# Kernel optimization log

Measured on AMD Instinct MI355X. Metric: run time of the kernel, lower is better.

The kernel has to match this reference:

```python
import jax, jax.numpy as jnp
import numpy as np

N = 8192      # nodes
E = 131072    # edges (avg degree 16)
MUL = 128     # multiplicity of 0e and 1o channels
A = 10        # node_attrs (element one-hot) dim
RB = 8        # radial basis size
INV_SQRT3 = 0.5773502691896258  # w3j normalization for l=1 paths


def _lin0(x, W):
    # e3nn-style Linear on scalar (l=0) channels, 1/sqrt(fan_in) normalization
    return (x @ W) / jnp.sqrt(jnp.asarray(W.shape[0], x.dtype))


def _lin1(v, W):
    # e3nn-style Linear on l=1 channels: mixes multiplicities, acts identically on the 3 components
    return jnp.einsum('nuc,uw->nwc', v, W) / jnp.sqrt(jnp.asarray(W.shape[0], v.dtype))


def setup_inputs() -> dict:
    key = jax.random.key(0)
    ks = jax.random.split(key, 26)
    f32 = jnp.float32
    w = lambda k, s: jax.random.normal(k, s, f32)
    D_EF = RB + 2 * MUL  # 264: radial basis + source + target scalar embeddings
    return {
        'node_attrs': jax.random.uniform(ks[0], (N, A), f32),
        'node_feats': w(ks[1], (N, 4 * MUL)),
        'edge_attrs': w(ks[2], (E, 4)),
        'edge_feats': jax.random.uniform(ks[3], (E, RB), f32),
        'edge_index': jax.random.randint(ks[4], (2, E), 0, N, jnp.int32),
        'W_skip_s': w(ks[5], (MUL, MUL)), 'W_skip_v': w(ks[6], (MUL, MUL)),
        'W_up_s': w(ks[7], (MUL, MUL)), 'W_up_v': w(ks[8], (MUL, MUL)),
        'W_src': w(ks[9], (A, MUL)), 'W_tgt': w(ks[10], (A, MUL)),
        'W_r0': w(ks[11], (D_EF, 64)), 'W_r1': w(ks[12], (64, 64)),
        'W_r2': w(ks[13], (64, 64)), 'W_r3': w(ks[14], (64, 4 * MUL)),
        'W_d0': w(ks[15], (D_EF, 64)), 'W_d1': w(ks[16], (64, 1)),
        'W1_s': w(ks[17], (2 * MUL, 2 * MUL)), 'W1_v': w(ks[18], (2 * MUL, MUL)),
        'Wres_s': w(ks[19], (MUL, 2 * MUL)), 'Wres_v': w(ks[20], (MUL, MUL)),
        'W2_s': w(ks[21], (MUL, MUL)), 'W2_v': w(ks[22], (MUL, MUL)),
        'alpha': jnp.asarray(20.0, f32), 'beta': jnp.asarray(0.0, f32),
    }


def reference(node_attrs, node_feats, edge_attrs, edge_feats, edge_index,
              W_skip_s, W_skip_v, W_up_s, W_up_v, W_src, W_tgt,
              W_r0, W_r1, W_r2, W_r3, W_d0, W_d1,
              W1_s, W1_v, Wres_s, Wres_v, W2_s, W2_v, alpha, beta):
    n = node_feats.shape[0]
    s = node_feats[:, :MUL]                       # [N,128] 0e
    v = node_feats[:, MUL:].reshape(n, MUL, 3)    # [N,128,3] 1o
    # skip_tp: Linear(node_feats -> hidden)
    sc = jnp.concatenate([_lin0(s, W_skip_s), _lin1(v, W_skip_v).reshape(n, -1)], axis=-1)
    # linear_up: Linear(node_feats -> edge_irreps)
    us, uv = _lin0(s, W_up_s), _lin1(v, W_up_v)
    # source/target scalar embeddings from node_attrs
    src_e = _lin0(node_attrs, W_src)
    tgt_e = _lin0(node_attrs, W_tgt)
    snd, rcv = edge_index[0], edge_index[1]
    ef = jnp.concatenate([edge_feats, src_e[snd], tgt_e[rcv]], axis=-1)   # [E,264]
    # radial MLP -> per-edge tensor product weights
    h = jax.nn.silu(_lin0(ef, W_r0))
    h = jax.nn.silu(_lin0(h, W_r1))
    h = jax.nn.silu(_lin0(h, W_r2))
    tpw = _lin0(h, W_r3)                          # [E, 4*128]
    # edge density -> per-node density via scatter-sum
    d = jax.nn.silu(_lin0(ef, W_d0))
    edge_density = jnp.tanh(_lin0(d, W_d1) ** 2)  # [E,1]
    density = jax.ops.segment_sum(edge_density, rcv, num_segments=n)      # [N,1]
    # sparse CG tensor product (uvu), paths: 0x0->0e, 0x1->1o, 1x0->1o, 1x1->0e
    xs, xv = us[snd], uv[snd]                     # gather sender features
    y0, y1 = edge_attrs[:, 0], edge_attrs[:, 1:4]
    w1, w2, w3, w4 = jnp.split(tpw, 4, axis=-1)
    m0a = w1 * xs * y0[:, None]                                          # 0e x 0e -> 0e
    m0b = w4 * jnp.einsum('euc,ec->eu', xv, y1) * INV_SQRT3              # 1o x 1o -> 0e
    m1a = (w2 * xs)[:, :, None] * y1[:, None, :] * INV_SQRT3             # 0e x 1o -> 1o
    m1b = w3[:, :, None] * xv * y0[:, None, None] * INV_SQRT3            # 1o x 0e -> 1o
    mid_s = jnp.concatenate([m0a, m0b], axis=1)   # [E,256] irreps_mid scalars
    mid_v = jnp.concatenate([m1a, m1b], axis=1)   # [E,256,3] irreps_mid vectors
    msg_s = jax.ops.segment_sum(mid_s, rcv, num_segments=n)
    msg_v = jax.ops.segment_sum(mid_v, rcv, num_segments=n)
    # linear_1 + learned density normalization
    denom = density * beta + alpha                # [N,1]
    m_s = _lin0(msg_s, W1_s) / denom
    m_v = _lin1(msg_v, W1_v) / denom[..., None]
    # linear_res on up-projected node feats
    m_s = m_s + _lin0(us, Wres_s)                 # [N,256]: 128 scalars + 128 gates
    m_v = m_v + _lin1(uv, Wres_v)                 # [N,128,3]
    # Gate: silu on scalars, sigmoid gates on vectors
    out_s = jax.nn.silu(m_s[:, :MUL])
    out_v = m_v * jax.nn.sigmoid(m_s[:, MUL:])[:, :, None]
    # linear_2
    f_s = _lin0(out_s, W2_s)
    f_v = _lin1(out_v, W2_v)
    # reshape_irreps -> [N, mul, 1+3]
    out = jnp.concatenate([f_s[:, :, None], f_v], axis=2)
    return out, sc
```

## Files before the change

### kernel.cpp

```cpp
#include <hip/hip_runtime.h>

#define NN 8192
#define EE 131072
#define MUL 128
#define AA 10
#define RB 8
#define DEF 264
#define INV_SQRT3 0.5773502691896258f
#define INV_SQRT128 0.08838834764831845f
#define INV_SQRT10 0.31622776601683794f
#define INV_SQRT264 0.06154574548966636f

typedef __attribute__((ext_vector_type(8))) short short8;
typedef __attribute__((ext_vector_type(4))) float floatx4;

#define WS_XQ     ((size_t)0)
#define WS_USB    (WS_XQ    + (size_t)NN*256)
#define WS_UVB    (WS_USB   + (size_t)NN*64)
#define WS_SRC    (WS_UVB   + (size_t)NN*192)
#define WS_TGT    (WS_SRC   + (size_t)NN*64)
#define WS_MSGSB  (WS_TGT   + (size_t)NN*64)
#define WS_MSGVB  (WS_MSGSB + (size_t)NN*128)
#define WS_GATE   (WS_MSGVB + (size_t)NN*384)
#define WS_COUNTS (WS_GATE  + (size_t)NN*128)
#define WS_OFFS   (WS_COUNTS+ (size_t)NN)
#define WS_CURSOR (WS_OFFS  + (size_t)(NN+4))
#define WS_POS    (WS_CURSOR+ (size_t)NN)
#define WS_META   (WS_POS   + (size_t)EE)
#define WS_TPW    (WS_META  + (size_t)EE*8)
#define WS_WB     (WS_TPW   + (size_t)EE*256)
#define WS_WP     (WS_WB    + (size_t)152*256)
#define WS_WN     (WS_WP    + (size_t)352*256)

__device__ __forceinline__ float silu_f(float x) { return x / (1.f + __expf(-x)); }
__device__ __forceinline__ float sigm_f(float x) { return 1.f / (1.f + __expf(-x)); }

__device__ __forceinline__ unsigned short f2bf(float x) {
    union { float f; unsigned u; } uf; uf.f = x;
    unsigned r = uf.u + 0x7FFFu + ((uf.u >> 16) & 1u);
    return (unsigned short)(r >> 16);
}

__global__ __launch_bounds__(256) void csr_count(
    const int* __restrict__ edge_index, int* __restrict__ counts)
{
    int e = blockIdx.x * 256 + threadIdx.x;
    atomicAdd(&counts[edge_index[EE + e]], 1);
}

__global__ __launch_bounds__(1024) void csr_scan(
    const int* __restrict__ counts, int* __restrict__ offs, int* __restrict__ cursor)
{
    __shared__ int sums[1024];
    const int t = threadIdx.x;
    int local[8];
    int s = 0;
#pragma unroll
    for (int k = 0; k < 8; ++k) { local[k] = s; s += counts[t * 8 + k]; }
    sums[t] = s;
    __syncthreads();
    for (int d = 1; d < 1024; d <<= 1) {
        int v = (t >= d) ? sums[t - d] : 0;
        __syncthreads();
        sums[t] += v;
        __syncthreads();
    }
    int base = (t > 0) ? sums[t - 1] : 0;
#pragma unroll
    for (int k = 0; k < 8; ++k) {
        offs[t * 8 + k] = base + local[k];
        cursor[t * 8 + k] = base + local[k];
    }
    if (t == 1023) offs[8192] = sums[1023];
}

__global__ __launch_bounds__(256) void csr_scatter(
    const int* __restrict__ edge_index, int* __restrict__ cursor, int* __restrict__ pos)
{
    int e = blockIdx.x * 256 + threadIdx.x;
    pos[e] = atomicAdd(&cursor[edge_index[EE + e]], 1);
}

__global__ __launch_bounds__(256) void swizzle_weights(
    const float* __restrict__ Wr0, const float* __restrict__ Wd0,
    const float* __restrict__ Wr1, const float* __restrict__ Wr2,
    const float* __restrict__ Wr3, unsigned short* __restrict__ WBall)
{
    int fid = blockIdx.x * 256 + threadIdx.x;
    int lane = fid & 63;
    int frag = fid >> 6;
    int k0 = (lane >> 4) * 8;
    int n0 = lane & 15;
    unsigned short o[8];

    if (frag < 72) {
        int kt = frag >> 3, nt = frag & 7;
        int n = nt * 16 + n0;
#pragma unroll
        for (int j = 0; j < 8; ++j) {
            int k = kt * 32 + k0 + j;
            float v = 0.f;
            if (k < 264) v = ((n < 64) ? Wr0[k * 64 + n] : Wd0[k * 64 + (n - 64)]) * INV_SQRT264;
            o[j] = f2bf(v);
        }
    } else if (frag < 80) {
        int fl = frag - 72;
        int kt = fl >> 2, nt = fl & 3;
        int n = nt * 16 + n0;
#pragma unroll
        for (int j = 0; j < 8; ++j)
            o[j] = f2bf(Wr1[(kt * 32 + k0 + j) * 64 + n] * 0.125f);
    } else if (frag < 88) {
        int fl = frag - 80;
        int kt = fl >> 2, nt = fl & 3;
        int n = nt * 16 + n0;
#pragma unroll
        for (int j = 0; j < 8; ++j)
            o[j] = f2bf(Wr2[(kt * 32 + k0 + j) * 64 + n] * 0.125f);
    } else {
        int fl = frag - 88;
        int kt = fl >> 5, nt = fl & 31;
        int n = nt * 16 + n0;
        int q = n >> 6;
        float sc = (q < 2) ? 0.125f : 0.125f * INV_SQRT3;
#pragma unroll
        for (int j = 0; j < 8; ++j)
            o[j] = f2bf(Wr3[(kt * 32 + k0 + j) * 512 + n] * sc);
    }
    uint4 pk;
    pk.x = (unsigned)o[0] | ((unsigned)o[1] << 16);
    pk.y = (unsigned)o[2] | ((unsigned)o[3] << 16);
    pk.z = (unsigned)o[4] | ((unsigned)o[5] << 16);
    pk.w = (unsigned)o[6] | ((unsigned)o[7] << 16);
    *(uint4*)(WBall + (size_t)fid * 8) = pk;
}

__global__ __launch_bounds__(256) void swizzle_post(
    const float* __restrict__ W1s, const float* __restrict__ W1v,
    const float* __restrict__ Wrs, const float* __restrict__ Wrv,
    const float* __restrict__ W2s, const float* __restrict__ W2v,
    unsigned short* __restrict__ WPall)
{
    int fid = blockIdx.x * 256 + threadIdx.x;
    int lane = fid & 63;
    int frag = fid >> 6;
    int k0 = (lane >> 4) * 8;
    int n0 = lane & 15;
    unsigned short o[8];

    if (frag < 192) {
        int kt = frag >> 4, nt = frag & 15;
        int n = nt * 16 + n0;
#pragma unroll
        for (int j = 0; j < 8; ++j) {
            int k = kt * 32 + k0 + j;
            float v = (k < 256) ? W1s[k * 256 + n] * 0.0625f
                                : Wrs[(k - 256) * 256 + n] * INV_SQRT128;
            o[j] = f2bf(v);
        }
    } else if (frag < 288) {
        int fl = frag - 192;
        int kt = fl >> 3, nt = fl & 7;
        int n = nt * 16 + n0;
#pragma unroll
        for (int j = 0; j < 8; ++j) {
            int k = kt * 32 + k0 + j;
            float v = (k < 256) ? W1v[k * 128 + n] * 0.0625f
                                : Wrv[(k - 256) * 128 + n] * INV_SQRT128;
            o[j] = f2bf(v);
        }
    } else if (frag < 320) {
        int fl = frag - 288;
        int kt = fl >> 3, nt = fl & 7;
        int n = nt * 16 + n0;
#pragma unroll
        for (int j = 0; j < 8; ++j)
            o[j] = f2bf(W2s[(kt * 32 + k0 + j) * 128 + n] * INV_SQRT128);
    } else {
        int fl = frag - 320;
        int kt = fl >> 3, nt = fl & 7;
        int n = nt * 16 + n0;
#pragma unroll
        for (int j = 0; j < 8; ++j)
            o[j] = f2bf(W2v[(kt * 32 + k0 + j) * 128 + n] * INV_SQRT128);
    }
    uint4 pk;
    pk.x = (unsigned)o[0] | ((unsigned)o[1] << 16);
    pk.y = (unsigned)o[2] | ((unsigned)o[3] << 16);
    pk.z = (unsigned)o[4] | ((unsigned)o[5] << 16);
    pk.w = (unsigned)o[6] | ((unsigned)o[7] << 16);
    *(uint4*)(WPall + (size_t)fid * 8) = pk;
}

__global__ __launch_bounds__(256) void swizzle_node(
    const float* __restrict__ Wss, const float* __restrict__ Wus,
    const float* __restrict__ Wsv, const float* __restrict__ Wuv,
    const float* __restrict__ Wsrc, const float* __restrict__ Wtgt,
    unsigned short* __restrict__ WN)
{
    int fid = blockIdx.x * 256 + threadIdx.x;
    int lane = fid & 63;
    int frag = fid >> 6;
    int k0 = (lane >> 4) * 8;
    int m0 = lane & 15;
    unsigned short o[8];

    if (frag < 128) {
        int g = frag >> 5;
        int fl = frag & 31;
        int kt = fl >> 3, mt = fl & 7;
        const float* W = (g == 0) ? Wss : (g == 1) ? Wus : (g == 2) ? Wsv : Wuv;
        int m = mt * 16 + m0;
#pragma unroll
        for (int j = 0; j < 8; ++j)
            o[j] = f2bf(W[(kt * 32 + k0 + j) * 128 + m] * INV_SQRT128);
    } else {
        int g = (frag - 128) >> 3;
        int mt = frag & 7;
        const float* W = g ? Wtgt : Wsrc;
        int m = mt * 16 + m0;
#pragma unroll
        for (int j = 0; j < 8; ++j) {
            int k = k0 + j;
            o[j] = f2bf((k < AA) ? W[k * 128 + m] * INV_SQRT10 : 0.f);
        }
    }
    uint4 pk;
    pk.x = (unsigned)o[0] | ((unsigned)o[1] << 16);
    pk.y = (unsigned)o[2] | ((unsigned)o[3] << 16);
    pk.z = (unsigned)o[4] | ((unsigned)o[5] << 16);
    pk.w = (unsigned)o[6] | ((unsigned)o[7] << 16);
    *(uint4*)(WN + (size_t)fid * 8) = pk;
}

#define PNB 16
__global__ __launch_bounds__(256) void node_pre_mfma(
    const float* __restrict__ node_attrs, const float* __restrict__ node_feats,
    const unsigned short* __restrict__ WN,
    float* __restrict__ sc_out, uint2* __restrict__ xq,
    unsigned short* __restrict__ us_b, unsigned short* __restrict__ uv_b,
    unsigned short* __restrict__ srcEb, unsigned short* __restrict__ tgtEb)
{
    __shared__ __align__(16) unsigned short Xs[PNB][136];
    __shared__ __align__(16) unsigned short Xv[3][PNB][136];
    __shared__ __align__(16) unsigned short Xa[PNB][40];
    const int t = threadIdx.x;
    const int l = t & 63, w = t >> 6;
    const int quad = l >> 4, lr = l & 15;
    const int n0 = blockIdx.x * PNB;

    {
        const int r = t >> 4, m = t & 15;
        const float* src = node_feats + (size_t)(n0 + r) * 512;
        float4 s0 = *(const float4*)(src + 8 * m);
        float4 s1 = *(const float4*)(src + 8 * m + 4);
        uint4 sp;
        sp.x = (unsigned)f2bf(s0.x) | ((unsigned)f2bf(s0.y) << 16);
        sp.y = (unsigned)f2bf(s0.z) | ((unsigned)f2bf(s0.w) << 16);
        sp.z = (unsigned)f2bf(s1.x) | ((unsigned)f2bf(s1.y) << 16);
        sp.w = (unsigned)f2bf(s1.z) | ((unsigned)f2bf(s1.w) << 16);
        *(uint4*)&Xs[r][8 * m] = sp;

        float4 q[6];
#pragma unroll
        for (int jj = 0; jj < 6; ++jj)
            q[jj] = *(const float4*)(src + 128 + 24 * m + 4 * jj);
        const float* qf = &q[0].x;
        unsigned short vb[3][8];
#pragma unroll
        for (int u = 0; u < 8; ++u) {
#pragma unroll
            for (int c = 0; c < 3; ++c)
                vb[c][u] = f2bf(qf[u * 3 + c]);
        }
#pragma unroll
        for (int c = 0; c < 3; ++c) {
            uint4 vp;
            vp.x = (unsigned)vb[c][0] | ((unsigned)vb[c][1] << 16);
            vp.y = (unsigned)vb[c][2] | ((unsigned)vb[c][3] << 16);
            vp.z = (unsigned)vb[c][4] | ((unsigned)vb[c][5] << 16);
            vp.w = (unsigned)vb[c][6] | ((unsigned)vb[c][7] << 16);
            *(uint4*)&Xv[c][r][8 * m] = vp;
        }
    }
    for (int idx = t; idx < PNB * 32; idx += 256) {
        int r = idx >> 5, k = idx & 31;
        float v = (k < AA) ? node_attrs[(size_t)(n0 + r) * AA + k] : 0.f;
        Xa[r][k] = f2bf(v);
    }
    __syncthreads();

    const short8* WNf = (const short8*)WN;
    const int n = n0 + lr;

#pragma unroll
    for (int mi = 0; mi < 2; ++mi) {
        const int mt = w * 2 + mi;
        const int j0 = mt * 16 + quad * 4;

        floatx4 cSrc = (floatx4){0.f, 0.f, 0.f, 0.f};
        floatx4 cTgt = (floatx4){0.f, 0.f, 0.f, 0.f};
        {
            short8 ba = *(const short8*)&Xa[lr][quad * 8];
            cSrc = __builtin_amdgcn_mfma_f32_16x16x32_bf16(WNf[(size_t)(128 + mt) * 64 + l], ba, cSrc, 0, 0, 0);
            cTgt = __builtin_amdgcn_mfma_f32_16x16x32_bf16(WNf[(size_t)(136 + mt) * 64 + l], ba, cTgt, 0, 0, 0);
        }
        floatx4 cS = (floatx4){0.f, 0.f, 0.f, 0.f};
        floatx4 cU = (floatx4){0.f, 0.f, 0.f, 0.f};
#pragma unroll
        for (int kt = 0; kt < 4; ++kt) {
            short8 bs = *(const short8*)&Xs[lr][kt * 32 + quad * 8];
            cS = __builtin_amdgcn_mfma_f32_16x16x32_bf16(WNf[(size_t)(kt * 8 + mt) * 64 + l], bs, cS, 0, 0, 0);
            cU = __builtin_amdgcn_mfma_f32_16x16x32_bf16(WNf[(size_t)(32 + kt * 8 + mt) * 64 + l], bs, cU, 0, 0, 0);
        }
        floatx4 cSV[3], cUV[3];
#pragma unroll
        for (int c = 0; c < 3; ++c) {
            cSV[c] = (floatx4){0.f, 0.f, 0.f, 0.f};
            cUV[c] = (floatx4){0.f, 0.f, 0.f, 0.f};
#pragma unroll
            for (int kt = 0; kt < 4; ++kt) {
                short8 bv = *(const short8*)&Xv[c][lr][kt * 32 + quad * 8];
                cSV[c] = __builtin_amdgcn_mfma_f32_16x16x32_bf16(WNf[(size_t)(64 + kt * 8 + mt) * 64 + l], bv, cSV[c], 0, 0, 0);
                cUV[c] = __builtin_amdgcn_mfma_f32_16x16x32_bf16(WNf[(size_t)(96 + kt * 8 + mt) * 64 + l], bv, cUV[c], 0, 0, 0);
            }
        }

        {
            float4 o;
            o.x = cS[0]; o.y = cS[1]; o.z = cS[2]; o.w = cS[3];
            *(float4*)(sc_out + (size_t)n * 512 + j0) = o;
        }
        {
            float vv[12];
#pragma unroll
            for (int reg = 0; reg < 4; ++reg)
#pragma unroll
                for (int c = 0; c < 3; ++c) vv[reg * 3 + c] = cSV[c][reg];
            float* dst = sc_out + (size_t)n * 512 + 128 + j0 * 3;
#pragma unroll
            for (int qq = 0; qq < 3; ++qq) {
                float4 o;
                o.x = vv[qq * 4]; o.y = vv[qq * 4 + 1]; o.z = vv[qq * 4 + 2]; o.w = vv[qq * 4 + 3];
                *(float4*)(dst + qq * 4) = o;
            }
        }
        unsigned short ub[4], vxb[4], vyb[4], vzb[4];
#pragma unroll
        for (int reg = 0; reg < 4; ++reg) {
            ub[reg] = f2bf(cU[reg]);
            vxb[reg] = f2bf(cUV[0][reg]);
            vyb[reg] = f2bf(cUV[1][reg]);
            vzb[reg] = f2bf(cUV[2][reg]);
        }
        {
            uint2 p;
            p.x = (unsigned)ub[0] | ((unsigned)ub[1] << 16);
            p.y = (unsigned)ub[2] | ((unsigned)ub[3] << 16);
            *(uint2*)(us_b + (size_t)n * 128 + j0) = p;
        }
        {
            uint2 p;
            p.x = (unsigned)vxb[0] | ((unsigned)vxb[1] << 16);
            p.y = (unsigned)vxb[2] | ((unsigned)vxb[3] << 16);
            *(uint2*)(uv_b + ((size_t)0 * NN + n) * 128 + j0) = p;
            p.x = (unsigned)vyb[0] | ((unsigned)vyb[1] << 16);
            p.y = (unsigned)vyb[2] | ((unsigned)vyb[3] << 16);
            *(uint2*)(uv_b + ((size_t)1 * NN + n) * 128 + j0) = p;
            p.x = (unsigned)vzb[0] | ((unsigned)vzb[1] << 16);
            p.y = (unsigned)vzb[2] | ((unsigned)vzb[3] << 16);
            *(uint2*)(uv_b + ((size_t)2 * NN + n) * 128 + j0) = p;
        }
        {
            uint4 x0, x1;
            x0.x = (unsigned)ub[0] | ((unsigned)vxb[0] << 16);
            x0.y = (unsigned)vyb[0] | ((unsigned)vzb[0] << 16);
            x0.z = (unsigned)ub[1] | ((unsigned)vxb[1] << 16);
            x0.w = (unsigned)vyb[1] | ((unsigned)vzb[1] << 16);
            x1.x = (unsigned)ub[2] | ((unsigned)vxb[2] << 16);
            x1.y = (unsigned)vyb[2] | ((unsigned)vzb[2] << 16);
            x1.z = (unsigned)ub[3] | ((unsigned)vxb[3] << 16);
            x1.w = (unsigned)vyb[3] | ((unsigned)vzb[3] << 16);
            uint4* xp = (uint4*)(xq + (size_t)n * 128 + j0);
            xp[0] = x0; xp[1] = x1;
        }
        {
            uint2 p;
            p.x = (unsigned)f2bf(cSrc[0]) | ((unsigned)f2bf(cSrc[1]) << 16);
            p.y = (unsigned)f2bf(cSrc[2]) | ((unsigned)f2bf(cSrc[3]) << 16);
            *(uint2*)(srcEb + (size_t)n * 128 + j0) = p;
            p.x = (unsigned)f2bf(cTgt[0]) | ((unsigned)f2bf(cTgt[1]) << 16);
            p.y = (unsigned)f2bf(cTgt[2]) | ((unsigned)f2bf(cTgt[3]) << 16);
            *(uint2*)(tgtEb + (size_t)n * 128 + j0) = p;
        }
    }
}

#define EBK 64
#define H1OFF 80
__global__ __launch_bounds__(256) void edge_mlp(
    const float* __restrict__ edge_attrs, const float* __restrict__ edge_feats,
    const int* __restrict__ edge_index,
    const unsigned short* __restrict__ srcEb, const unsigned short* __restrict__ tgtEb,
    const unsigned short* __restrict__ WB0, const unsigned short* __restrict__ WB1,
    const unsigned short* __restrict__ WB2, const unsigned short* __restrict__ WB3,
    const float* __restrict__ Wd1, const int* __restrict__ pos,
    unsigned short* __restrict__ tpwP, float* __restrict__ metaP)
{
    __shared__ __align__(16) unsigned short efb[EBK][296];
    __shared__ int snd_l[EBK], rcv_l[EBK], slot_l[EBK];
    __shared__ float y_l[EBK][4];

    const int t = threadIdx.x;
    const int l = t & 63;
    const int w = t >> 6;
    const int quad = l >> 4;
    const int lr = l & 15;
    const int e0 = blockIdx.x * EBK;

    if (t < EBK) {
        snd_l[t] = edge_index[e0 + t];
        rcv_l[t] = edge_index[EE + e0 + t];
        slot_l[t] = pos[e0 + t];
    }
    __syncthreads();

    if (t < EBK) {
        float4 ya = *(const float4*)(edge_attrs + (size_t)(e0 + t) * 4);
        y_l[t][0] = ya.x; y_l[t][1] = ya.y; y_l[t][2] = ya.z; y_l[t][3] = ya.w;
        float4 m;
        m.x = __int_as_float(snd_l[t]); m.y = ya.y; m.z = ya.z; m.w = ya.w;
        *(float4*)(metaP + (size_t)slot_l[t] * 8) = m;
        float4 f0 = *(const float4*)(edge_feats + (size_t)(e0 + t) * 8);
        float4 f1 = *(const float4*)(edge_feats + (size_t)(e0 + t) * 8 + 4);
        uint4 o;
        o.x = (unsigned)f2bf(f0.x) | ((unsigned)f2bf(f0.y) << 16);
        o.y = (unsigned)f2bf(f0.z) | ((unsigned)f2bf(f0.w) << 16);
        o.z = (unsigned)f2bf(f1.x) | ((unsigned)f2bf(f1.y) << 16);
        o.w = (unsigned)f2bf(f1.z) | ((unsigned)f2bf(f1.w) << 16);
        *(uint4*)&efb[t][0] = o;
    }
    for (int idx = t; idx < EBK * 16; idx += 256) {
        int e = idx >> 4, c = idx & 15;
        *(uint4*)&efb[e][8 + c * 8] =
            *(const uint4*)(srcEb + (size_t)snd_l[e] * 128 + c * 8);
        *(uint4*)&efb[e][136 + c * 8] =
            *(const uint4*)(tgtEb + (size_t)rcv_l[e] * 128 + c * 8);
    }
    for (int idx = t; idx < EBK * 3; idx += 256) {
        int e = idx / 3, c = idx - e * 3;
        uint4 z; z.x = 0; z.y = 0; z.z = 0; z.w = 0;
        *(uint4*)&efb[e][264 + c * 8] = z;
    }
    __syncthreads();

    const int rb = w * 16;
    int rowr[4], slotr[4];
    float y0r[4];
#pragma unroll
    for (int reg = 0; reg < 4; ++reg) {
        rowr[reg] = rb + quad * 4 + reg;
        slotr[reg] = slot_l[rowr[reg]];
        y0r[reg] = y_l[rowr[reg]][0];
    }
    float wd1v[4];
#pragma unroll
    for (int q2 = 0; q2 < 4; ++q2) wd1v[q2] = Wd1[q2 * 16 + lr] * 0.125f;

    floatx4 c0[8];
#pragma unroll
    for (int nt = 0; nt < 8; ++nt) c0[nt] = (floatx4){0.f, 0.f, 0.f, 0.f};
    const unsigned short* arow = &efb[rb + lr][quad * 8];
#pragma unroll
    for (int kt = 0; kt < 9; ++kt) {
        short8 af = *(const short8*)(arow + kt * 32);
        const short8* bp = (const short8*)WB0 + (size_t)(kt * 8) * 64 + l;
#pragma unroll
        for (int nt = 0; nt < 8; ++nt) {
            short8 bf = bp[nt * 64];
            c0[nt] = __builtin_amdgcn_mfma_f32_16x16x32_bf16(af, bf, c0[nt], 0, 0, 0);
        }
    }
    float dp[4] = {0.f, 0.f, 0.f, 0.f};
#pragma unroll
    for (int nt = 0; nt < 4; ++nt) {
#pragma unroll
        for (int reg = 0; reg < 4; ++reg) {
            efb[rowr[reg]][nt * 16 + lr] = f2bf(silu_f(c0[nt][reg]));
            dp[reg] += silu_f(c0[nt + 4][reg]) * wd1v[nt];
        }
    }
#pragma unroll
    for (int m2 = 1; m2 < 16; m2 <<= 1) {
#pragma unroll
        for (int reg = 0; reg < 4; ++reg) dp[reg] += __shfl_xor(dp[reg], m2);
    }
    if (lr == 0) {
#pragma unroll
        for (int reg = 0; reg < 4; ++reg)
            metaP[(size_t)slotr[reg] * 8 + 4] = tanhf(dp[reg] * dp[reg]);
    }

    const unsigned short* hrow0 = &efb[rb + lr][quad * 8];
    const unsigned short* hrow1 = &efb[rb + lr][H1OFF + quad * 8];

    {
        floatx4 c1[4];
#pragma unroll
        for (int nt = 0; nt < 4; ++nt) c1[nt] = (floatx4){0.f, 0.f, 0.f, 0.f};
#pragma unroll
        for (int kt = 0; kt < 2; ++kt) {
            short8 af = *(const short8*)(hrow0 + kt * 32);
            const short8* bp = (const short8*)WB1 + (size_t)(kt * 4) * 64 + l;
#pragma unroll
            for (int nt = 0; nt < 4; ++nt)
                c1[nt] = __builtin_amdgcn_mfma_f32_16x16x32_bf16(af, bp[nt * 64], c1[nt], 0, 0, 0);
        }
#pragma unroll
        for (int nt = 0; nt < 4; ++nt)
#pragma unroll
            for (int reg = 0; reg < 4; ++reg)
                efb[rowr[reg]][H1OFF + nt * 16 + lr] = f2bf(silu_f(c1[nt][reg]));
    }

    {
        floatx4 c2[4];
#pragma unroll
        for (int nt = 0; nt < 4; ++nt) c2[nt] = (floatx4){0.f, 0.f, 0.f, 0.f};
#pragma unroll
        for (int kt = 0; kt < 2; ++kt) {
            short8 af = *(const short8*)(hrow1 + kt * 32);
            const short8* bp = (const short8*)WB2 + (size_t)(kt * 4) * 64 + l;
#pragma unroll
            for (int nt = 0; nt < 4; ++nt)
                c2[nt] = __builtin_amdgcn_mfma_f32_16x16x32_bf16(af, bp[nt * 64], c2[nt], 0, 0, 0);
        }
#pragma unroll
        for (int nt = 0; nt < 4; ++nt)
#pragma unroll
            for (int reg = 0; reg < 4; ++reg)
                efb[rowr[reg]][nt * 16 + lr] = f2bf(silu_f(c2[nt][reg]));
    }

    {
        short8 af0 = *(const short8*)(hrow0);
        short8 af1 = *(const short8*)(hrow0 + 32);
        uint2* tpw2 = (uint2*)tpwP;
#pragma unroll
        for (int j2 = 0; j2 < 8; ++j2) {
            floatx4 c3[4];
#pragma unroll
            for (int g = 0; g < 4; ++g) c3[g] = (floatx4){0.f, 0.f, 0.f, 0.f};
#pragma unroll
            for (int g = 0; g < 4; ++g) {
                const short8* b0 = (const short8*)WB3 + (size_t)(g * 8 + j2) * 64 + l;
                const short8* b1 = (const short8*)WB3 + (size_t)(32 + g * 8 + j2) * 64 + l;
                c3[g] = __builtin_amdgcn_mfma_f32_16x16x32_bf16(af0, *b0, c3[g], 0, 0, 0);
                c3[g] = __builtin_amdgcn_mfma_f32_16x16x32_bf16(af1, *b1, c3[g], 0, 0, 0);
            }
            const int u = j2 * 16 + lr;
#pragma unroll
            for (int reg = 0; reg < 4; ++reg) {
                float w1v = c3[0][reg] * y0r[reg];
                float w2v = c3[1][reg];
                float w3v = c3[2][reg] * y0r[reg];
                float w4v = c3[3][reg];
                uint2 p;
                p.x = (unsigned)f2bf(w1v) | ((unsigned)f2bf(w2v) << 16);
                p.y = (unsigned)f2bf(w3v) | ((unsigned)f2bf(w4v) << 16);
                tpw2[(size_t)slotr[reg] * 128 + u] = p;
            }
        }
    }
}

__global__ __launch_bounds__(128) void node_gather(
    const unsigned short* __restrict__ tpwP, const float* __restrict__ metaP,
    const int* __restrict__ offs, const uint2* __restrict__ xq,
    const float* __restrict__ alpha_p, const float* __restrict__ beta_p,
    unsigned short* __restrict__ msgs_b, unsigned short* __restrict__ msgv_b)
{
    const int n = blockIdx.x;
    const int j = threadIdx.x;
    const int s0 = offs[n], s1 = offs[n + 1];
    const uint2* tpw2 = (const uint2*)tpwP;

    float as0 = 0.f, as1 = 0.f;
    float av0x = 0.f, av0y = 0.f, av0z = 0.f;
    float av1x = 0.f, av1y = 0.f, av1z = 0.f;
    float dsum = 0.f;

    int s = s0;
    for (; s + 4 <= s1; s += 4) {
        float4 ma[4]; float dn[4]; uint2 wv[4]; uint2 xv[4];
#pragma unroll
        for (int k = 0; k < 4; ++k) {
            ma[k] = *(const float4*)&metaP[(size_t)(s + k) * 8];
            dn[k] = metaP[(size_t)(s + k) * 8 + 4];
            wv[k] = tpw2[(size_t)(s + k) * 128 + j];
        }
#pragma unroll
        for (int k = 0; k < 4; ++k)
            xv[k] = xq[(size_t)__float_as_int(ma[k].x) * 128 + j];
#pragma unroll
        for (int k = 0; k < 4; ++k) {
            const float y1x = ma[k].y, y1y = ma[k].z, y1z = ma[k].w;
            dsum += dn[k];
            const float w1  = __uint_as_float(wv[k].x << 16);
            const float w2  = __uint_as_float(wv[k].x & 0xffff0000u);
            const float w3  = __uint_as_float(wv[k].y << 16);
            const float w4  = __uint_as_float(wv[k].y & 0xffff0000u);
            const float xs  = __uint_as_float(xv[k].x << 16);
            const float xvx = __uint_as_float(xv[k].x & 0xffff0000u);
            const float xvy = __uint_as_float(xv[k].y << 16);
            const float xvz = __uint_as_float(xv[k].y & 0xffff0000u);
            as0 += w1 * xs;
            as1 += w4 * (xvx * y1x + xvy * y1y + xvz * y1z);
            const float b2 = w2 * xs;
            av0x += b2 * y1x; av0y += b2 * y1y; av0z += b2 * y1z;
            av1x += w3 * xvx; av1y += w3 * xvy; av1z += w3 * xvz;
        }
    }
    for (; s < s1; ++s) {
        const float4 m0 = *(const float4*)&metaP[(size_t)s * 8];
        const float dns = metaP[(size_t)s * 8 + 4];
        const int snd = __float_as_int(m0.x);
        const float y1x = m0.y, y1y = m0.z, y1z = m0.w;
        dsum += dns;
        uint2 wv = tpw2[(size_t)s * 128 + j];
        uint2 xv = xq[(size_t)snd * 128 + j];
        const float w1  = __uint_as_float(wv.x << 16);
        const float w2  = __uint_as_float(wv.x & 0xffff0000u);
        const float w3  = __uint_as_float(wv.y << 16);
        const float w4  = __uint_as_float(wv.y & 0xffff0000u);
        const float xs  = __uint_as_float(xv.x << 16);
        const float xvx = __uint_as_float(xv.x & 0xffff0000u);
        const float xvy = __uint_as_float(xv.y << 16);
        const float xvz = __uint_as_float(xv.y & 0xffff0000u);
        as0 += w1 * xs;
        as1 += w4 * (xvx * y1x + xvy * y1y + xvz * y1z);
        const float b2 = w2 * xs;
        av0x += b2 * y1x; av0y += b2 * y1y; av0z += b2 * y1z;
        av1x += w3 * xvx; av1y += w3 * xvy; av1z += w3 * xvz;
    }

    const float invden = 1.f / (dsum * (*beta_p) + (*alpha_p));

    msgs_b[(size_t)n * 256 + j]       = f2bf(as0 * invden);
    msgs_b[(size_t)n * 256 + 128 + j] = f2bf(as1 * invden);
    msgv_b[((size_t)0 * NN + n) * 256 + j]       = f2bf(av0x * invden);
    msgv_b[((size_t)0 * NN + n) * 256 + 128 + j] = f2bf(av1x * invden);
    msgv_b[((size_t)1 * NN + n) * 256 + j]       = f2bf(av0y * invden);
    msgv_b[((size_t)1 * NN + n) * 256 + 128 + j] = f2bf(av1y * invden);
    msgv_b[((size_t)2 * NN + n) * 256 + j]       = f2bf(av0z * invden);
    msgv_b[((size_t)2 * NN + n) * 256 + 128 + j] = f2bf(av1z * invden);
}

#define DNP 32
__global__ __launch_bounds__(256) void post_s(
    const unsigned short* __restrict__ msgs_b, const unsigned short* __restrict__ us_b,
    const unsigned short* __restrict__ WPs, const unsigned short* __restrict__ W2ss,
    float* __restrict__ gate, float* __restrict__ out)
{
    __shared__ __align__(16) unsigned short At[DNP][392];
    __shared__ __align__(16) unsigned short osb[DNP][136];
    const int t = threadIdx.x;
    const int l = t & 63, w = t >> 6;
    const int quad = l >> 4, lr = l & 15;
    const int n0 = blockIdx.x * DNP;
    const int rt = w & 1, nh = w >> 1;

    for (int idx = t; idx < DNP * 48; idx += 256) {
        int r = idx / 48, q = idx - r * 48;
        uint4 v;
        if (q < 32) v = *(const uint4*)(msgs_b + (size_t)(n0 + r) * 256 + q * 8);
        else        v = *(const uint4*)(us_b   + (size_t)(n0 + r) * 128 + (q - 32) * 8);
        *(uint4*)&At[r][q * 8] = v;
    }
    __syncthreads();

    int rowr[4];
#pragma unroll
    for (int reg = 0; reg < 4; ++reg) rowr[reg] = rt * 16 + quad * 4 + reg;

    floatx4 c1[8];
#pragma unroll
    for (int nt = 0; nt < 8; ++nt) c1[nt] = (floatx4){0.f, 0.f, 0.f, 0.f};
    const unsigned short* arow = &At[rt * 16 + lr][quad * 8];
#pragma unroll
    for (int kt = 0; kt < 12; ++kt) {
        short8 af = *(const short8*)(arow + kt * 32);
        const short8* bp = (const short8*)WPs + (size_t)(kt * 16 + nh * 8) * 64 + l;
#pragma unroll
        for (int nt = 0; nt < 8; ++nt)
            c1[nt] = __builtin_amdgcn_mfma_f32_16x16x32_bf16(af, bp[nt * 64], c1[nt], 0, 0, 0);
    }
    if (nh == 0) {
#pragma unroll
        for (int nt = 0; nt < 8; ++nt)
#pragma unroll
            for (int reg = 0; reg < 4; ++reg)
                osb[rowr[reg]][nt * 16 + lr] = f2bf(silu_f(c1[nt][reg]));
    } else {
#pragma unroll
        for (int nt = 0; nt < 8; ++nt)
#pragma unroll
            for (int reg = 0; reg < 4; ++reg)
                gate[(size_t)(n0 + rowr[reg]) * 128 + nt * 16 + lr] = sigm_f(c1[nt][reg]);
    }
    __syncthreads();

    floatx4 c2[4];
#pragma unroll
    for (int nt = 0; nt < 4; ++nt) c2[nt] = (floatx4){0.f, 0.f, 0.f, 0.f};
    const unsigned short* arow2 = &osb[rt * 16 + lr][quad * 8];
#pragma unroll
    for (int kt = 0; kt < 4; ++kt) {
        short8 af = *(const short8*)(arow2 + kt * 32);
        const short8* bp = (const short8*)W2ss + (size_t)(kt * 8 + nh * 4) * 64 + l;
#pragma unroll
        for (int nt = 0; nt < 4; ++nt)
            c2[nt] = __builtin_amdgcn_mfma_f32_16x16x32_bf16(af, bp[nt * 64], c2[nt], 0, 0, 0);
    }
#pragma unroll
    for (int nt = 0; nt < 4; ++nt)
#pragma unroll
        for (int reg = 0; reg < 4; ++reg)
            out[(size_t)(n0 + rowr[reg]) * 512 + (nh * 64 + nt * 16 + lr) * 4] = c2[nt][reg];
}

__global__ __launch_bounds__(256) void post_v(
    const unsigned short* __restrict__ msgv_b, const unsigned short* __restrict__ uv_b,
    const unsigned short* __restrict__ WPv, const unsigned short* __restrict__ W2vs,
    const float* __restrict__ gate, float* __restrict__ out)
{
    __shared__ __align__(16) unsigned short At[DNP][392];
    __shared__ __align__(16) unsigned short ovb[DNP][136];
    const int t = threadIdx.x;
    const int l = t & 63, w = t >> 6;
    const int quad = l >> 4, lr = l & 15;
    const int c = blockIdx.x >> 8;
    const int n0 = (blockIdx.x & 255) * DNP;
    const int rt = w & 1, nh = w >> 1;

    for (int idx = t; idx < DNP * 48; idx += 256) {
        int r = idx / 48, q = idx - r * 48;
        uint4 v;
        if (q < 32) v = *(const uint4*)(msgv_b + ((size_t)c * NN + n0 + r) * 256 + q * 8);
        else        v = *(const uint4*)(uv_b   + ((size_t)c * NN + n0 + r) * 128 + (q - 32) * 8);
        *(uint4*)&At[r][q * 8] = v;
    }
    __syncthreads();

    int rowr[4];
#pragma unroll
    for (int reg = 0; reg < 4; ++reg) rowr[reg] = rt * 16 + quad * 4 + reg;

    floatx4 c1[4];
#pragma unroll
    for (int nt = 0; nt < 4; ++nt) c1[nt] = (floatx4){0.f, 0.f, 0.f, 0.f};
    const unsigned short* arow = &At[rt * 16 + lr][quad * 8];
#pragma unroll
    for (int kt = 0; kt < 12; ++kt) {
        short8 af = *(const short8*)(arow + kt * 32);
        const short8* bp = (const short8*)WPv + (size_t)(kt * 8 + nh * 4) * 64 + l;
#pragma unroll
        for (int nt = 0; nt < 4; ++nt)
            c1[nt] = __builtin_amdgcn_mfma_f32_16x16x32_bf16(af, bp[nt * 64], c1[nt], 0, 0, 0);
    }
#pragma unroll
    for (int nt = 0; nt < 4; ++nt)
#pragma unroll
        for (int reg = 0; reg < 4; ++reg) {
            int col = nh * 64 + nt * 16 + lr;
            float g = gate[(size_t)(n0 + rowr[reg]) * 128 + col];
            ovb[rowr[reg]][col] = f2bf(c1[nt][reg] * g);
        }
    __syncthreads();

    floatx4 c2[4];
#pragma unroll
    for (int nt = 0; nt < 4; ++nt) c2[nt] = (floatx4){0.f, 0.f, 0.f, 0.f};
    const unsigned short* arow2 = &ovb[rt * 16 + lr][quad * 8];
#pragma unroll
    for (int kt = 0; kt < 4; ++kt) {
        short8 af = *(const short8*)(arow2 + kt * 32);
        const short8* bp = (const short8*)W2vs + (size_t)(kt * 8 + nh * 4) * 64 + l;
#pragma unroll
        for (int nt = 0; nt < 4; ++nt)
            c2[nt] = __builtin_amdgcn_mfma_f32_16x16x32_bf16(af, bp[nt * 64], c2[nt], 0, 0, 0);
    }
#pragma unroll
    for (int nt = 0; nt < 4; ++nt)
#pragma unroll
        for (int reg = 0; reg < 4; ++reg)
            out[(size_t)(n0 + rowr[reg]) * 512 + (nh * 64 + nt * 16 + lr) * 4 + 1 + c]
                = c2[nt][reg];
}

extern "C" void kernel_launch(void* const* d_in, const int* in_sizes, int n_in,
                              void* d_out, int out_size, void* d_ws, size_t ws_size,
                              hipStream_t stream)
{
    const float* node_attrs = (const float*)d_in[0];
    const float* node_feats = (const float*)d_in[1];
    const float* edge_attrs = (const float*)d_in[2];
    const float* edge_feats = (const float*)d_in[3];
    const int*   edge_index = (const int*)d_in[4];
    const float* W_skip_s = (const float*)d_in[5];
    const float* W_skip_v = (const float*)d_in[6];
    const float* W_up_s   = (const float*)d_in[7];
    const float* W_up_v   = (const float*)d_in[8];
    const float* W_src    = (const float*)d_in[9];
    const float* W_tgt    = (const float*)d_in[10];
    const float* W_r0     = (const float*)d_in[11];
    const float* W_r1     = (const float*)d_in[12];
    const float* W_r2     = (const float*)d_in[13];
    const float* W_r3     = (const float*)d_in[14];
    const float* W_d0     = (const float*)d_in[15];
    const float* W_d1     = (const float*)d_in[16];
    const float* W1_s     = (const float*)d_in[17];
    const float* W1_v     = (const float*)d_in[18];
    const float* Wres_s   = (const float*)d_in[19];
    const float* Wres_v   = (const float*)d_in[20];
    const float* W2_s     = (const float*)d_in[21];
    const float* W2_v     = (const float*)d_in[22];
    const float* alpha_p  = (const float*)d_in[23];
    const float* beta_p   = (const float*)d_in[24];

    float* out = (float*)d_out;
    float* sc_out = out + (size_t)NN * 512;
    float* ws = (float*)d_ws;

    uint2* xq = (uint2*)(ws + WS_XQ);
    unsigned short* us_b  = (unsigned short*)(ws + WS_USB);
    unsigned short* uv_b  = (unsigned short*)(ws + WS_UVB);
    unsigned short* srcEb = (unsigned short*)(ws + WS_SRC);
    unsigned short* tgtEb = (unsigned short*)(ws + WS_TGT);
    unsigned short* msgs_b = (unsigned short*)(ws + WS_MSGSB);
    unsigned short* msgv_b = (unsigned short*)(ws + WS_MSGVB);
    float* gate  = ws + WS_GATE;
    int*   counts = (int*)(ws + WS_COUNTS);
    int*   offs   = (int*)(ws + WS_OFFS);
    int*   cursor = (int*)(ws + WS_CURSOR);
    int*   pos    = (int*)(ws + WS_POS);
    float* metaP  = ws + WS_META;
    unsigned short* tpwP = (unsigned short*)(ws + WS_TPW);
    unsigned short* WBall = (unsigned short*)(ws + WS_WB);
    unsigned short* WB0 = WBall;
    unsigned short* WB1 = WB0 + (size_t)72 * 512;
    unsigned short* WB2 = WB1 + (size_t)8 * 512;
    unsigned short* WB3 = WB2 + (size_t)8 * 512;
    unsigned short* WPall = (unsigned short*)(ws + WS_WP);
    unsigned short* WPs  = WPall;
    unsigned short* WPv  = WPs + (size_t)192 * 512;
    unsigned short* W2ss = WPv + (size_t)96 * 512;
    unsigned short* W2vs = W2ss + (size_t)32 * 512;
    unsigned short* WN   = (unsigned short*)(ws + WS_WN);

    hipMemsetAsync(counts, 0, (size_t)NN * sizeof(int), stream);

    csr_count<<<EE / 256, 256, 0, stream>>>(edge_index, counts);
    csr_scan<<<1, 1024, 0, stream>>>(counts, offs, cursor);
    csr_scatter<<<EE / 256, 256, 0, stream>>>(edge_index, cursor, pos);

    swizzle_weights<<<38, 256, 0, stream>>>(W_r0, W_d0, W_r1, W_r2, W_r3, WBall);
    swizzle_post<<<88, 256, 0, stream>>>(W1_s, W1_v, Wres_s, Wres_v, W2_s, W2_v, WPall);
    swizzle_node<<<36, 256, 0, stream>>>(W_skip_s, W_up_s, W_skip_v, W_up_v,
                                         W_src, W_tgt, WN);

    node_pre_mfma<<<NN / PNB, 256, 0, stream>>>(
        node_attrs, node_feats, WN, sc_out, xq, us_b, uv_b, srcEb, tgtEb);

    edge_mlp<<<EE / EBK, 256, 0, stream>>>(
        edge_attrs, edge_feats, edge_index, srcEb, tgtEb,
        WB0, WB1, WB2, WB3, W_d1, pos, tpwP, metaP);

    node_gather<<<NN, 128, 0, stream>>>(
        tpwP, metaP, offs, xq, alpha_p, beta_p, msgs_b, msgv_b);

    post_s<<<NN / DNP, 256, 0, stream>>>(msgs_b, us_b, WPs, W2ss, gate, out);
    post_v<<<3 * NN / DNP, 256, 0, stream>>>(msgv_b, uv_b, WPv, W2vs, gate, out);
}
```

Baseline: 317.9 us.

## Load edge MLP A-fragments directly into registers, shrink LDS to per-wave buffers

The edge MLP no longer stages the gathered 264-wide edge features in a block-wide shared buffer. Each lane now loads its bf16 A-fragments straight from the source/target embeddings into registers, and shared memory drops to a small per-wave hidden buffer. This removes the block-level barriers and cuts LDS use. The first layer is split into two passes of four N-tiles to limit accumulator registers, and launch bounds request 8 blocks per CU. silu and sigmoid now use the hardware reciprocal instead of a divide. The trade-off is more register pressure from holding nine fragments, plus uncoalesced per-lane global gathers and some repeated pos/edge_attrs loads.

```diff
diff --git a/kernel.cpp b/kernel.cpp
--- a/kernel.cpp
+++ b/kernel.cpp
@@ -32,8 +32,12 @@
 #define WS_WP     (WS_WB    + (size_t)152*256)
 #define WS_WN     (WS_WP    + (size_t)352*256)
 
-__device__ __forceinline__ float silu_f(float x) { return x / (1.f + __expf(-x)); }
-__device__ __forceinline__ float sigm_f(float x) { return 1.f / (1.f + __expf(-x)); }
+__device__ __forceinline__ float silu_f(float x) {
+    return x * __builtin_amdgcn_rcpf(1.f + __expf(-x));
+}
+__device__ __forceinline__ float sigm_f(float x) {
+    return __builtin_amdgcn_rcpf(1.f + __expf(-x));
+}
 
 __device__ __forceinline__ unsigned short f2bf(float x) {
     union { float f; unsigned u; } uf; uf.f = x;
@@ -398,7 +402,8 @@
 
 #define EBK 64
 #define H1OFF 80
-__global__ __launch_bounds__(256) void edge_mlp(
+#define HLD 152
+__global__ __launch_bounds__(256, 8) void edge_mlp(
     const float* __restrict__ edge_attrs, const float* __restrict__ edge_feats,
     const int* __restrict__ edge_index,
     const unsigned short* __restrict__ srcEb, const unsigned short* __restrict__ tgtEb,
@@ -407,102 +412,111 @@
     const float* __restrict__ Wd1, const int* __restrict__ pos,
     unsigned short* __restrict__ tpwP, float* __restrict__ metaP)
 {
-    __shared__ __align__(16) unsigned short efb[EBK][296];
-    __shared__ int snd_l[EBK], rcv_l[EBK], slot_l[EBK];
-    __shared__ float y_l[EBK][4];
+    __shared__ __align__(16) unsigned short Hb[4][16][HLD];
 
     const int t = threadIdx.x;
     const int l = t & 63;
     const int w = t >> 6;
     const int quad = l >> 4;
     const int lr = l & 15;
-    const int e0 = blockIdx.x * EBK;
-
-    if (t < EBK) {
-        snd_l[t] = edge_index[e0 + t];
-        rcv_l[t] = edge_index[EE + e0 + t];
-        slot_l[t] = pos[e0 + t];
-    }
-    __syncthreads();
-
-    if (t < EBK) {
-        float4 ya = *(const float4*)(edge_attrs + (size_t)(e0 + t) * 4);
-        y_l[t][0] = ya.x; y_l[t][1] = ya.y; y_l[t][2] = ya.z; y_l[t][3] = ya.w;
+    const int e0 = blockIdx.x * EBK + w * 16;
+
+    const int eA = e0 + lr;
+    const int sndA = edge_index[eA];
+    const int rcvA = edge_index[EE + eA];
+    const unsigned short* spp = srcEb + (size_t)sndA * 128;
+    const unsigned short* tpp = tgtEb + (size_t)rcvA * 128;
+
+    if (quad == 0) {
+        float4 ya = *(const float4*)(edge_attrs + (size_t)eA * 4);
         float4 m;
-        m.x = __int_as_float(snd_l[t]); m.y = ya.y; m.z = ya.z; m.w = ya.w;
-        *(float4*)(metaP + (size_t)slot_l[t] * 8) = m;
-        float4 f0 = *(const float4*)(edge_feats + (size_t)(e0 + t) * 8);
-        float4 f1 = *(const float4*)(edge_feats + (size_t)(e0 + t) * 8 + 4);
-        uint4 o;
-        o.x = (unsigned)f2bf(f0.x) | ((unsigned)f2bf(f0.y) << 16);
-        o.y = (unsigned)f2bf(f0.z) | ((unsigned)f2bf(f0.w) << 16);
-        o.z = (unsigned)f2bf(f1.x) | ((unsigned)f2bf(f1.y) << 16);
-        o.w = (unsigned)f2bf(f1.z) | ((unsigned)f2bf(f1.w) << 16);
-        *(uint4*)&efb[t][0] = o;
-    }
-    for (int idx = t; idx < EBK * 16; idx += 256) {
-        int e = idx >> 4, c = idx & 15;
-        *(uint4*)&efb[e][8 + c * 8] =
-            *(const uint4*)(srcEb + (size_t)snd_l[e] * 128 + c * 8);
-        *(uint4*)&efb[e][136 + c * 8] =
-            *(const uint4*)(tgtEb + (size_t)rcv_l[e] * 128 + c * 8);
-    }
-    for (int idx = t; idx < EBK * 3; idx += 256) {
-        int e = idx / 3, c = idx - e * 3;
-        uint4 z; z.x = 0; z.y = 0; z.z = 0; z.w = 0;
-        *(uint4*)&efb[e][264 + c * 8] = z;
-    }
-    __syncthreads();
-
-    const int rb = w * 16;
-    int rowr[4], slotr[4];
-    float y0r[4];
-#pragma unroll
-    for (int reg = 0; reg < 4; ++reg) {
-        rowr[reg] = rb + quad * 4 + reg;
-        slotr[reg] = slot_l[rowr[reg]];
-        y0r[reg] = y_l[rowr[reg]][0];
-    }
-    float wd1v[4];
-#pragma unroll
-    for (int q2 = 0; q2 < 4; ++q2) wd1v[q2] = Wd1[q2 * 16 + lr] * 0.125f;
-
-    floatx4 c0[8];
-#pragma unroll
-    for (int nt = 0; nt < 8; ++nt) c0[nt] = (floatx4){0.f, 0.f, 0.f, 0.f};
-    const unsigned short* arow = &efb[rb + lr][quad * 8];
-#pragma unroll
-    for (int kt = 0; kt < 9; ++kt) {
-        short8 af = *(const short8*)(arow + kt * 32);
-        const short8* bp = (const short8*)WB0 + (size_t)(kt * 8) * 64 + l;
-#pragma unroll
-        for (int nt = 0; nt < 8; ++nt) {
-            short8 bf = bp[nt * 64];
-            c0[nt] = __builtin_amdgcn_mfma_f32_16x16x32_bf16(af, bf, c0[nt], 0, 0, 0);
-        }
-    }
-    float dp[4] = {0.f, 0.f, 0.f, 0.f};
-#pragma unroll
-    for (int nt = 0; nt < 4; ++nt) {
-#pragma unroll
-        for (int reg = 0; reg < 4; ++reg) {
-            efb[rowr[reg]][nt * 16 + lr] = f2bf(silu_f(c0[nt][reg]));
-            dp[reg] += silu_f(c0[nt + 4][reg]) * wd1v[nt];
-        }
-    }
-#pragma unroll
-    for (int m2 = 1; m2 < 16; m2 <<= 1) {
-#pragma unroll
-        for (int reg = 0; reg < 4; ++reg) dp[reg] += __shfl_xor(dp[reg], m2);
-    }
-    if (lr == 0) {
-#pragma unroll
-        for (int reg = 0; reg < 4; ++reg)
-            metaP[(size_t)slotr[reg] * 8 + 4] = tanhf(dp[reg] * dp[reg]);
-    }
-
-    const unsigned short* hrow0 = &efb[rb + lr][quad * 8];
-    const unsigned short* hrow1 = &efb[rb + lr][H1OFF + quad * 8];
+        m.x = __int_as_float(sndA); m.y = ya.y; m.z = ya.z; m.w = ya.w;
+        *(float4*)(metaP + (size_t)pos[eA] * 8) = m;
+    }
+
+    short8 afr[9];
+    {
+        const int cq = quad * 8;
+        if (quad == 0) {
+            float4 f0 = *(const float4*)(edge_feats + (size_t)eA * 8);
+            float4 f1 = *(const float4*)(edge_feats + (size_t)eA * 8 + 4);
+            union { short8 v; unsigned u[4]; } pk;
+            pk.u[0] = (unsigned)f2bf(f0.x) | ((unsigned)f2bf(f0.y) << 16);
+            pk.u[1] = (unsigned)f2bf(f0.z) | ((unsigned)f2bf(f0.w) << 16);
+            pk.u[2] = (unsigned)f2bf(f1.x) | ((unsigned)f2bf(f1.y) << 16);
+            pk.u[3] = (unsigned)f2bf(f1.z) | ((unsigned)f2bf(f1.w) << 16);
+            afr[0] = pk.v;
+        } else {
+            afr[0] = *(const short8*)(spp + (cq - 8));
+        }
+#pragma unroll
+        for (int kt = 1; kt < 9; ++kt) {
+            const int c = kt * 32 + cq;
+            if (c < 136) {
+                afr[kt] = *(const short8*)(spp + (c - 8));
+            } else if (c < 264) {
+                afr[kt] = *(const short8*)(tpp + (c - 136));
+            } else {
+                short8 z = {0, 0, 0, 0, 0, 0, 0, 0};
+                afr[kt] = z;
+            }
+        }
+    }
+
+    unsigned short (*H)[HLD] = Hb[w];
+
+    {
+        floatx4 cr[4];
+#pragma unroll
+        for (int nt = 0; nt < 4; ++nt) cr[nt] = (floatx4){0.f, 0.f, 0.f, 0.f};
+#pragma unroll
+        for (int kt = 0; kt < 9; ++kt) {
+            const short8* bp = (const short8*)WB0 + (size_t)(kt * 8) * 64 + l;
+#pragma unroll
+            for (int nt = 0; nt < 4; ++nt)
+                cr[nt] = __builtin_amdgcn_mfma_f32_16x16x32_bf16(afr[kt], bp[nt * 64], cr[nt], 0, 0, 0);
+        }
+#pragma unroll
+        for (int nt = 0; nt < 4; ++nt)
+#pragma unroll
+            for (int reg = 0; reg < 4; ++reg)
+                H[quad * 4 + reg][nt * 16 + lr] = f2bf(silu_f(cr[nt][reg]));
+    }
+
+    {
+        floatx4 cd[4];
+#pragma unroll
+        for (int nt = 0; nt < 4; ++nt) cd[nt] = (floatx4){0.f, 0.f, 0.f, 0.f};
+#pragma unroll
+        for (int kt = 0; kt < 9; ++kt) {
+            const short8* bp = (const short8*)WB0 + (size_t)(kt * 8 + 4) * 64 + l;
+#pragma unroll
+            for (int nt = 0; nt < 4; ++nt)
+                cd[nt] = __builtin_amdgcn_mfma_f32_16x16x32_bf16(afr[kt], bp[nt * 64], cd[nt], 0, 0, 0);
+        }
+        float wd1v[4];
+#pragma unroll
+        for (int q2 = 0; q2 < 4; ++q2) wd1v[q2] = Wd1[q2 * 16 + lr] * 0.125f;
+        float dp[4] = {0.f, 0.f, 0.f, 0.f};
+#pragma unroll
+        for (int nt = 0; nt < 4; ++nt)
+#pragma unroll
+            for (int reg = 0; reg < 4; ++reg)
+                dp[reg] += silu_f(cd[nt][reg]) * wd1v[nt];
+#pragma unroll
+        for (int m2 = 1; m2 < 16; m2 <<= 1) {
+#pragma unroll
+            for (int reg = 0; reg < 4; ++reg) dp[reg] += __shfl_xor(dp[reg], m2);
+        }
+        if (lr == 0) {
+#pragma unroll
+            for (int reg = 0; reg < 4; ++reg)
+                metaP[(size_t)pos[e0 + quad * 4 + reg] * 8 + 4] = tanhf(dp[reg] * dp[reg]);
+        }
+    }
+
+    const unsigned short* hrow0 = &H[lr][quad * 8];
+    const unsigned short* hrow1 = &H[lr][H1OFF + quad * 8];
 
     {
         floatx4 c1[4];
@@ -520,7 +534,7 @@
         for (int nt = 0; nt < 4; ++nt)
 #pragma unroll
             for (int reg = 0; reg < 4; ++reg)
-                efb[rowr[reg]][H1OFF + nt * 16 + lr] = f2bf(silu_f(c1[nt][reg]));
+                H[quad * 4 + reg][H1OFF + nt * 16 + lr] = f2bf(silu_f(c1[nt][reg]));
     }
 
     {
@@ -539,10 +553,18 @@
         for (int nt = 0; nt < 4; ++nt)
 #pragma unroll
             for (int reg = 0; reg < 4; ++reg)
-                efb[rowr[reg]][nt * 16 + lr] = f2bf(silu_f(c2[nt][reg]));
+                H[quad * 4 + reg][nt * 16 + lr] = f2bf(silu_f(c2[nt][reg]));
     }
 
     {
+        int slotr[4];
+        float y0r[4];
+#pragma unroll
+        for (int reg = 0; reg < 4; ++reg) {
+            const int er = e0 + quad * 4 + reg;
+            slotr[reg] = pos[er];
+            y0r[reg] = edge_attrs[(size_t)er * 4];
+        }
         short8 af0 = *(const short8*)(hrow0);
         short8 af1 = *(const short8*)(hrow0 + 32);
         uint2* tpw2 = (uint2*)tpwP;
```

New measurement: 380.8 us. 1.2x slower.
